# Kernel optimization log

Measured on AMD Instinct MI355X. Metric: run time of the kernel, lower is better.

The kernel has to match this reference:

```python
import jax, jax.numpy as jnp
import numpy as np

GROUPS = 32
EPS = 1e-5


def group_norm(x, w, b):
    B, C, H, W = x.shape
    xg = x.reshape(B, GROUPS, C // GROUPS, H, W)
    mu = xg.mean(axis=(2, 3, 4), keepdims=True)
    var = xg.var(axis=(2, 3, 4), keepdims=True)
    xg = (xg - mu) * jax.lax.rsqrt(var + EPS)
    return xg.reshape(B, C, H, W) * w[None, :, None, None] + b[None, :, None, None]


def conv1x1(x, w, b):
    # 1x1 conv == per-position GEMM over channels
    return jnp.einsum('bchw,dc->bdhw', x, w) + b[None, :, None, None]


def setup_inputs() -> dict:
    key = jax.random.key(0)
    ks = jax.random.split(key, 8)
    B, C, H, W = 16, 512, 32, 32
    scale = C ** -0.5  # keep pre-softmax logits well-conditioned
    return {
        'x': jax.random.normal(ks[0], (B, C, H, W), jnp.float32),
        'temb': jax.random.normal(ks[1], (B, C), jnp.float32),
        'gn_w': jnp.ones((C,), jnp.float32),
        'gn_b': jnp.zeros((C,), jnp.float32),
        'q_w': jax.random.normal(ks[2], (C, C), jnp.float32) * scale,
        'q_b': jnp.zeros((C,), jnp.float32),
        'k_w': jax.random.normal(ks[3], (C, C), jnp.float32) * scale,
        'k_b': jnp.zeros((C,), jnp.float32),
        'v_w': jax.random.normal(ks[4], (C, C), jnp.float32) * scale,
        'v_b': jnp.zeros((C,), jnp.float32),
        'p_w': jax.random.normal(ks[5], (C, C), jnp.float32) * scale,
        'p_b': jnp.zeros((C,), jnp.float32),
    }


def reference(x, temb, gn_w, gn_b, q_w, q_b, k_w, k_b, v_w, v_b, p_w, p_b):
    B, C, H, W = x.shape
    h = group_norm(x, gn_w, gn_b)
    q = conv1x1(h, q_w, q_b)
    k = conv1x1(h, k_w, k_b)
    v = conv1x1(h, v_w, v_b)
    # spatial self-attention: every (h,w) query attends over all (H,W) keys
    scores = jnp.einsum('bchw,bcHW->bhwHW', q, k) * (C ** -0.5)  # [B,H,W,H,W]
    attn = jax.nn.softmax(scores.reshape(B, H, W, H * W), axis=-1).reshape(B, H, W, H, W)
    h = jnp.einsum('bhwHW,bcHW->bchw', attn, v)
    return x + conv1x1(h, p_w, p_b)
```

## Files before the change

kernel.cpp:

```cpp
#include <hip/hip_runtime.h>

typedef unsigned short u16;
typedef __bf16 bf16x8 __attribute__((ext_vector_type(8)));
typedef float f32x4 __attribute__((ext_vector_type(4)));
typedef unsigned short u16x8 __attribute__((ext_vector_type(8)));

__device__ __forceinline__ u16 f2bf(float f) {
  unsigned u = __builtin_bit_cast(unsigned, f);
  u += 0x7fffu + ((u >> 16) & 1u);
  return (u16)(u >> 16);
}
__device__ __forceinline__ float b2f(u16 h) {
  return __builtin_bit_cast(float, (unsigned)h << 16);
}

__device__ __forceinline__ void async16(const void* g, void* l) {
  __builtin_amdgcn_global_load_lds((const __attribute__((address_space(1))) void*)g,
                                   (__attribute__((address_space(3))) void*)l, 16, 0, 0);
}

__global__ __launch_bounds__(256) void cvt_kernel(const float* __restrict__ qw, const float* __restrict__ kw,
                                                  const float* __restrict__ vw, const float* __restrict__ pw,
                                                  const float* __restrict__ qb, const float* __restrict__ kb,
                                                  u16* __restrict__ wqk, u16* __restrict__ wv,
                                                  u16* __restrict__ wp, float* __restrict__ qkb,
                                                  float scale) {
  if (blockIdx.y == 4) {
    int i = blockIdx.x * 256 + threadIdx.x;
    if (i < 512) qkb[i] = qb[i] * scale;
    else if (i < 1024) qkb[i] = kb[i - 512];
    return;
  }
  const float* s;
  u16* o;
  float sc = 1.f;
  switch (blockIdx.y) {
    case 0: s = qw; o = wqk; sc = scale; break;
    case 1: s = kw; o = wqk + 262144; break;
    case 2: s = vw; o = wv; break;
    default: s = pw; o = wp; break;
  }
  int i = (blockIdx.x * 256 + threadIdx.x) * 4;
  float4 v = *(const float4*)(s + i);
  ushort4 pk = { f2bf(v.x * sc), f2bf(v.y * sc), f2bf(v.z * sc), f2bf(v.w * sc) };
  *(ushort4*)&o[i] = pk;
}

#define GN_ROW 1026

__global__ __launch_bounds__(256) void gn_kernel(const float* __restrict__ x, const float* __restrict__ w,
                                                 const float* __restrict__ bias, u16* __restrict__ hn) {
  __shared__ u16 tile[16 * GN_ROW];
  __shared__ float red[18];
  const int tid = threadIdx.x;
  const int bb = blockIdx.x >> 5;
  const int g = blockIdx.x & 31;
  const float4* xb = (const float4*)(x + ((size_t)bb * 512 + (size_t)g * 16) * 1024);

  float s = 0.f, sq = 0.f;
#pragma unroll
  for (int j = 0; j < 16; ++j) {
    float4 v = xb[j * 256 + tid];
    s += v.x + v.y + v.z + v.w;
    sq += v.x * v.x + v.y * v.y + v.z * v.z + v.w * v.w;
    int base = j * GN_ROW + tid * 4;
    ushort2 p0 = { f2bf(v.x), f2bf(v.y) };
    ushort2 p1 = { f2bf(v.z), f2bf(v.w) };
    *(ushort2*)&tile[base] = p0;
    *(ushort2*)&tile[base + 2] = p1;
  }
#pragma unroll
  for (int o = 32; o; o >>= 1) {
    s += __shfl_down(s, o, 64);
    sq += __shfl_down(sq, o, 64);
  }
  const int wv = tid >> 6;
  if ((tid & 63) == 0) { red[wv] = s; red[wv + 4] = sq; }
  __syncthreads();
  if (tid == 0) {
    float S = red[0] + red[1] + red[2] + red[3];
    float Q = red[4] + red[5] + red[6] + red[7];
    float mean = S * (1.f / 16384.f);
    float var = Q * (1.f / 16384.f) - mean * mean;
    red[16] = mean;
    red[17] = rsqrtf(var + 1e-5f);
  }
  __syncthreads();
  const float mean = red[16], rstd = red[17];
  const int c0 = g * 16;

  float wf[16], bf_[16];
#pragma unroll
  for (int c = 0; c < 16; ++c) {
    float wc = w[c0 + c];
    wf[c] = wc * rstd;
    bf_[c] = bias[c0 + c] - mean * rstd * wc;
  }
#pragma unroll
  for (int it = 0; it < 4; ++it) {
    int hw = it * 256 + tid;
    u16x8 lo{}, hi{};
#pragma unroll
    for (int c = 0; c < 8; ++c) {
      lo[c] = f2bf(b2f(tile[c * GN_ROW + hw]) * wf[c] + bf_[c]);
      hi[c] = f2bf(b2f(tile[(c + 8) * GN_ROW + hw]) * wf[c + 8] + bf_[c + 8]);
    }
    u16* dst = hn + ((size_t)bb * 1024 + hw) * 512 + c0;
    *(u16x8*)dst = lo;
    *(u16x8*)(dst + 8) = hi;
  }
}

template <typename OutT>
__global__ __launch_bounds__(256) void gemm_nt(const u16* __restrict__ A, const u16* __restrict__ Bt,
                                               OutT* __restrict__ C, const float* __restrict__ bias_m,
                                               const float* __restrict__ bias_n, const float* __restrict__ res,
                                               int K, int lda, int ldb, int ldc,
                                               size_t sA, size_t sB, size_t sC, size_t sRes,
                                               int T, int lognbx) {
  __shared__ u16 lsA[128 * 64];
  __shared__ u16 lsB[128 * 64];
  int fi = blockIdx.x;
  const int halfT = T << 3;
  const int h = (fi >= halfT);
  fi -= h * halfT;
  const int tile = fi >> 3;
  const int zb = (fi & 7) + (h << 3);
  const int bx = tile & ((1 << lognbx) - 1);
  const int by = tile >> lognbx;

  const int tid = threadIdx.x;
  const int lane = tid & 63;
  const int wave = tid >> 6;
  const int wm = wave >> 1, wn = wave & 1;
  const int tm = by * 128, tn = bx * 128;
  const u16* Ab = A + (size_t)zb * sA;
  const u16* Bb = Bt + (size_t)zb * sB;

  f32x4 acc[4][4] = {};
  const int q = lane >> 4, r = lane & 15;

  int srow[4], gch[4];
#pragma unroll
  for (int i = 0; i < 4; ++i) {
    int e = tid + i * 256;
    srow[i] = e >> 3;
    gch[i] = (e & 7) ^ (srow[i] & 7);
  }

  for (int k0 = 0; k0 < K; k0 += 64) {
    __syncthreads();
#pragma unroll
    for (int i = 0; i < 4; ++i) {
      async16(Ab + (size_t)(tm + srow[i]) * lda + k0 + gch[i] * 8, (char*)lsA + (tid + i * 256) * 16);
      async16(Bb + (size_t)(tn + srow[i]) * ldb + k0 + gch[i] * 8, (char*)lsB + (tid + i * 256) * 16);
    }
    __syncthreads();

#pragma unroll
    for (int kk = 0; kk < 2; ++kk) {
      bf16x8 af[4], bfv[4];
#pragma unroll
      for (int mt = 0; mt < 4; ++mt) {
        int row = wm * 64 + mt * 16 + r;
        int chunk = (kk * 4 + q) ^ (row & 7);
        af[mt] = *(const bf16x8*)(const void*)&lsA[row * 64 + chunk * 8];
      }
#pragma unroll
      for (int nt = 0; nt < 4; ++nt) {
        int row = wn * 64 + nt * 16 + r;
        int chunk = (kk * 4 + q) ^ (row & 7);
        bfv[nt] = *(const bf16x8*)(const void*)&lsB[row * 64 + chunk * 8];
      }
#pragma unroll
      for (int mt = 0; mt < 4; ++mt)
#pragma unroll
        for (int nt = 0; nt < 4; ++nt)
          acc[mt][nt] = __builtin_amdgcn_mfma_f32_16x16x32_bf16(af[mt], bfv[nt], acc[mt][nt], 0, 0, 0);
    }
  }

  OutT* Cb = C + (size_t)zb * sC;
  const float* Rb = res ? res + (size_t)zb * sRes : nullptr;
#pragma unroll
  for (int mt = 0; mt < 4; ++mt) {
#pragma unroll
    for (int nt = 0; nt < 4; ++nt) {
      const int col = tn + wn * 64 + nt * 16 + r;
      const float bn = bias_n ? bias_n[col] : 0.f;
#pragma unroll
      for (int reg = 0; reg < 4; ++reg) {
        const int row = tm + wm * 64 + mt * 16 + q * 4 + reg;
        float v = acc[mt][nt][reg];
        const float bm = bias_m ? bias_m[row] : 0.f;
        v = v + bm + bn;
        const size_t idx = (size_t)row * ldc + col;
        if (Rb) v += Rb[idx];
        if constexpr (__is_same(OutT, u16)) Cb[idx] = f2bf(v);
        else Cb[idx] = v;
      }
    }
  }
}

__global__ __launch_bounds__(256) void softmax_kernel(u16* __restrict__ S) {
  const int row = blockIdx.x * 4 + (threadIdx.x >> 6);
  const int lane = threadIdx.x & 63;
  u16* p = S + (size_t)row * 1024;
  u16x8 a = *(const u16x8*)(p + lane * 8);
  u16x8 b = *(const u16x8*)(p + 512 + lane * 8);
  float va[8], vb[8];
  float m = -3.0e38f;
#pragma unroll
  for (int j = 0; j < 8; ++j) {
    va[j] = b2f(a[j]);
    vb[j] = b2f(b[j]);
    m = fmaxf(m, fmaxf(va[j], vb[j]));
  }
#pragma unroll
  for (int o = 32; o; o >>= 1) m = fmaxf(m, __shfl_xor(m, o, 64));
  float s = 0.f;
#pragma unroll
  for (int j = 0; j < 8; ++j) {
    va[j] = __expf(va[j] - m);
    vb[j] = __expf(vb[j] - m);
    s += va[j] + vb[j];
  }
#pragma unroll
  for (int o = 32; o; o >>= 1) s += __shfl_xor(s, o, 64);
  const float inv = 1.f / s;
  u16x8 oa, ob;
#pragma unroll
  for (int j = 0; j < 8; ++j) {
    oa[j] = f2bf(va[j] * inv);
    ob[j] = f2bf(vb[j] * inv);
  }
  *(u16x8*)(p + lane * 8) = oa;
  *(u16x8*)(p + 512 + lane * 8) = ob;
}

extern "C" void kernel_launch(void* const* d_in, const int* in_sizes, int n_in,
                              void* d_out, int out_size, void* d_ws, size_t ws_size,
                              hipStream_t stream) {
  const float* x = (const float*)d_in[0];
  const float* gn_w = (const float*)d_in[2];
  const float* gn_b = (const float*)d_in[3];
  const float* q_w = (const float*)d_in[4];
  const float* q_b = (const float*)d_in[5];
  const float* k_w = (const float*)d_in[6];
  const float* k_b = (const float*)d_in[7];
  const float* v_w = (const float*)d_in[8];
  const float* v_b = (const float*)d_in[9];
  const float* p_w = (const float*)d_in[10];
  const float* p_b = (const float*)d_in[11];
  float* out = (float*)d_out;

  u16* wqk = (u16*)d_ws;
  u16* wv = wqk + 524288;
  u16* wp = wv + 262144;
  float* qkb = (float*)(wp + 262144);
  u16* hn = wp + 262144 + 2048;
  u16* qkt = hn + 8388608;
  u16* vv = qkt + 16777216;
  u16* ot = vv + 8388608;
  u16* Sb = ot + 8388608;

  const float inv_sqrt_c = 0.044194173824159216f;
  const size_t sHN = 524288, sS = 1048576;

  cvt_kernel<<<dim3(256, 5), 256, 0, stream>>>(q_w, k_w, v_w, p_w, q_b, k_b, wqk, wv, wp, qkb, inv_sqrt_c);
  gn_kernel<<<512, 256, 0, stream>>>(x, gn_w, gn_b, hn);

  gemm_nt<u16><<<dim3(16 * 64), 256, 0, stream>>>(hn, wqk, qkt, nullptr, qkb, nullptr,
                                                  512, 512, 512, 1024, sHN, 0, sS, 0, 64, 3);
  gemm_nt<u16><<<dim3(16 * 32), 256, 0, stream>>>(wv, hn, vv, v_b, nullptr, nullptr,
                                                  512, 512, 512, 1024, 0, sHN, sHN, 0, 32, 3);
  gemm_nt<u16><<<dim3(16 * 64), 256, 0, stream>>>(qkt, qkt + 512, Sb, nullptr, nullptr, nullptr,
                                                  512, 1024, 1024, 1024, sS, sS, sS, 0, 64, 3);
  softmax_kernel<<<4096, 256, 0, stream>>>(Sb);
  gemm_nt<u16><<<dim3(16 * 32), 256, 0, stream>>>(Sb, vv, ot, nullptr, nullptr, nullptr,
                                                  1024, 1024, 1024, 512, sS, sHN, sHN, 0, 32, 2);
  gemm_nt<float><<<dim3(16 * 32), 256, 0, stream>>>(wp, ot, out, p_b, nullptr, x,
                                                    512, 512, 512, 1024, 0, sHN, sHN, sHN, 32, 3);
}
```

Measured before the change: 276.0 us.

## Load GEMM operands directly from global into registers with register prefetch

Drops the LDS staging in gemm_nt, including async global-to-LDS loads, swizzled shared tiles and barriers. Each wave now loads its own MFMA fragments straight from global memory and double-buffers them in registers one 32-wide k-step ahead. This removes LDS traffic and synchronisation. In exchange there is no data sharing between waves: each A/B fragment is fetched by two waves, so L2 traffic rises and the reads are narrower per row and less coalesced.

```diff
diff --git a/kernel.cpp b/kernel.cpp
--- a/kernel.cpp
+++ b/kernel.cpp
@@ -12,11 +12,6 @@
 }
 __device__ __forceinline__ float b2f(u16 h) {
   return __builtin_bit_cast(float, (unsigned)h << 16);
-}
-
-__device__ __forceinline__ void async16(const void* g, void* l) {
-  __builtin_amdgcn_global_load_lds((const __attribute__((address_space(1))) void*)g,
-                                   (__attribute__((address_space(3))) void*)l, 16, 0, 0);
 }
 
 __global__ __launch_bounds__(256) void cvt_kernel(const float* __restrict__ qw, const float* __restrict__ kw,
@@ -118,8 +113,6 @@
                                                int K, int lda, int ldb, int ldc,
                                                size_t sA, size_t sB, size_t sC, size_t sRes,
                                                int T, int lognbx) {
-  __shared__ u16 lsA[128 * 64];
-  __shared__ u16 lsB[128 * 64];
   int fi = blockIdx.x;
   const int halfT = T << 3;
   const int h = (fi >= halfT);
@@ -134,51 +127,52 @@
   const int wave = tid >> 6;
   const int wm = wave >> 1, wn = wave & 1;
   const int tm = by * 128, tn = bx * 128;
+  const int q = lane >> 4, r = lane & 15;
+
   const u16* Ab = A + (size_t)zb * sA;
   const u16* Bb = Bt + (size_t)zb * sB;
 
+  const u16* pa[4];
+  const u16* pb[4];
+#pragma unroll
+  for (int mt = 0; mt < 4; ++mt) {
+    pa[mt] = Ab + (size_t)(tm + wm * 64 + mt * 16 + r) * lda + q * 8;
+    pb[mt] = Bb + (size_t)(tn + wn * 64 + mt * 16 + r) * ldb + q * 8;
+  }
+
   f32x4 acc[4][4] = {};
-  const int q = lane >> 4, r = lane & 15;
-
-  int srow[4], gch[4];
+  bf16x8 ca[4], cb[4];
 #pragma unroll
   for (int i = 0; i < 4; ++i) {
-    int e = tid + i * 256;
-    srow[i] = e >> 3;
-    gch[i] = (e & 7) ^ (srow[i] & 7);
-  }
-
-  for (int k0 = 0; k0 < K; k0 += 64) {
-    __syncthreads();
+    ca[i] = *(const bf16x8*)(const void*)pa[i];
+    cb[i] = *(const bf16x8*)(const void*)pb[i];
+  }
+
+  const int nk = K >> 5;
+  for (int k = 1; k < nk; ++k) {
+    bf16x8 na[4], nb[4];
+    const int k0 = k << 5;
 #pragma unroll
     for (int i = 0; i < 4; ++i) {
-      async16(Ab + (size_t)(tm + srow[i]) * lda + k0 + gch[i] * 8, (char*)lsA + (tid + i * 256) * 16);
-      async16(Bb + (size_t)(tn + srow[i]) * ldb + k0 + gch[i] * 8, (char*)lsB + (tid + i * 256) * 16);
-    }
-    __syncthreads();
-
-#pragma unroll
-    for (int kk = 0; kk < 2; ++kk) {
-      bf16x8 af[4], bfv[4];
-#pragma unroll
-      for (int mt = 0; mt < 4; ++mt) {
-        int row = wm * 64 + mt * 16 + r;
-        int chunk = (kk * 4 + q) ^ (row & 7);
-        af[mt] = *(const bf16x8*)(const void*)&lsA[row * 64 + chunk * 8];
-      }
-#pragma unroll
-      for (int nt = 0; nt < 4; ++nt) {
-        int row = wn * 64 + nt * 16 + r;
-        int chunk = (kk * 4 + q) ^ (row & 7);
-        bfv[nt] = *(const bf16x8*)(const void*)&lsB[row * 64 + chunk * 8];
-      }
-#pragma unroll
-      for (int mt = 0; mt < 4; ++mt)
-#pragma unroll
-        for (int nt = 0; nt < 4; ++nt)
-          acc[mt][nt] = __builtin_amdgcn_mfma_f32_16x16x32_bf16(af[mt], bfv[nt], acc[mt][nt], 0, 0, 0);
-    }
-  }
+      na[i] = *(const bf16x8*)(const void*)(pa[i] + k0);
+      nb[i] = *(const bf16x8*)(const void*)(pb[i] + k0);
+    }
+#pragma unroll
+    for (int mt = 0; mt < 4; ++mt)
+#pragma unroll
+      for (int nt = 0; nt < 4; ++nt)
+        acc[mt][nt] = __builtin_amdgcn_mfma_f32_16x16x32_bf16(ca[mt], cb[nt], acc[mt][nt], 0, 0, 0);
+#pragma unroll
+    for (int i = 0; i < 4; ++i) {
+      ca[i] = na[i];
+      cb[i] = nb[i];
+    }
+  }
+#pragma unroll
+  for (int mt = 0; mt < 4; ++mt)
+#pragma unroll
+    for (int nt = 0; nt < 4; ++nt)
+      acc[mt][nt] = __builtin_amdgcn_mfma_f32_16x16x32_bf16(ca[mt], cb[nt], acc[mt][nt], 0, 0, 0);
 
   OutT* Cb = C + (size_t)zb * sC;
   const float* Rb = res ? res + (size_t)zb * sRes : nullptr;
```

After: 420.4 us. 52.3% more time.
